# Optimization experiments

Hardware: AMD Instinct MI355X
Metric: run time of the kernel (lower is better)

The kernel has to match this reference:

```python
import jax, jax.numpy as jnp
import numpy as np

B, S, P, D, H, L, DFF = 4, 2048, 32, 512, 8, 2, 2048
HD = D // H
NV = 8  # number of variates; S = NV * 256 patches
SCALE = 1.0 / np.sqrt(HD)


def _rope_tables(seq_len, dim, base=10000.0):
    inv = 1.0 / (base ** (jnp.arange(0, dim, 2, dtype=jnp.float32) / dim))
    freqs = jnp.outer(jnp.arange(seq_len, dtype=jnp.float32), inv)  # (S, dim/2)
    emb = jnp.concatenate([freqs, freqs], axis=-1)  # (S, dim)
    return jnp.cos(emb), jnp.sin(emb)


def _apply_rope(x, cos, sin):
    # x: (..., S, HD); cos/sin: (S, HD)
    x1, x2 = x[..., ::2], x[..., 1::2]
    ch, sh = cos[..., ::2], sin[..., ::2]
    r1 = x1 * ch - x2 * sh
    r2 = x1 * sh + x2 * ch
    return jnp.stack([r1, r2], axis=-1).reshape(x.shape)


def _ln(x, g, b, eps=1e-5):
    m = x.mean(-1, keepdims=True)
    v = x.var(-1, keepdims=True)
    return (x - m) / jnp.sqrt(v + eps) * g + b


def setup_inputs() -> dict:
    key = jax.random.key(0)
    ks = jax.random.split(key, 20)
    s = 0.02
    x = jax.random.normal(ks[0], (B, S, P), dtype=jnp.float32)
    # 8 variates, 256 patches each, flattened: [0]*256, [1]*256, ...
    variate_ids = jnp.broadcast_to(jnp.arange(S, dtype=jnp.int32) // (S // NV), (B, S))
    mask = jnp.ones((B, S), dtype=jnp.float32)
    f32 = jnp.float32
    return {
        'x': x, 'variate_ids': variate_ids, 'mask': mask,
        'W_pe': jax.random.normal(ks[1], (P, D), f32) * s, 'b_pe': jnp.zeros((D,), f32),
        'Wq': jax.random.normal(ks[2], (L, D, D), f32) * s, 'bq': jnp.zeros((L, D), f32),
        'Wk': jax.random.normal(ks[3], (L, D, D), f32) * s, 'bk': jnp.zeros((L, D), f32),
        'Wv': jax.random.normal(ks[4], (L, D, D), f32) * s, 'bv': jnp.zeros((L, D), f32),
        'Wo': jax.random.normal(ks[5], (L, D, D), f32) * s, 'bo': jnp.zeros((L, D), f32),
        'u_same': jax.random.normal(ks[6], (L, H), f32) * 0.1,
        'u_cross': jax.random.normal(ks[7], (L, H), f32) * 0.1,
        'g1': jnp.ones((L, D), f32), 'be1': jnp.zeros((L, D), f32),
        'W1': jax.random.normal(ks[8], (L, D, DFF), f32) * s, 'b1f': jnp.zeros((L, DFF), f32),
        'W2': jax.random.normal(ks[9], (L, DFF, D), f32) * s, 'b2f': jnp.zeros((L, D), f32),
        'g2': jnp.ones((L, D), f32), 'be2': jnp.zeros((L, D), f32),
        'Wh': jax.random.normal(ks[10], (D, P), f32) * s, 'bh': jnp.zeros((P,), f32),
    }


def reference(x, variate_ids, mask, W_pe, b_pe, Wq, bq, Wk, bk, Wv, bv, Wo, bo,
              u_same, u_cross, g1, be1, W1, b1f, W2, b2f, g2, be2, Wh, bh):
    b, s, _ = x.shape
    h = x @ W_pe + b_pe  # patch embedding: (B,S,D)
    cos, sin = _rope_tables(s, HD)
    same = (variate_ids[:, :, None] == variate_ids[:, None, :]).astype(h.dtype)  # (B,S,S)
    mask_add = (1.0 - mask)[:, None, None, :] * -1e9  # (B,1,1,S)
    for l in range(L):
        q = (h @ Wq[l] + bq[l]).reshape(b, s, H, HD).transpose(0, 2, 1, 3)
        k = (h @ Wk[l] + bk[l]).reshape(b, s, H, HD).transpose(0, 2, 1, 3)
        v = (h @ Wv[l] + bv[l]).reshape(b, s, H, HD).transpose(0, 2, 1, 3)
        q = _apply_rope(q, cos, sin)
        k = _apply_rope(k, cos, sin)
        scores = jnp.einsum('bhqd,bhkd->bhqk', q, k) * SCALE
        bias = (same[:, None] * u_same[l][None, :, None, None]
                + (1.0 - same)[:, None] * u_cross[l][None, :, None, None])
        scores = scores + bias + mask_add
        p = jax.nn.softmax(scores, axis=-1)
        o = jnp.einsum('bhqk,bhkd->bhqd', p, v).transpose(0, 2, 1, 3).reshape(b, s, D)
        o = o @ Wo[l] + bo[l]
        h = _ln(h + o, g1[l], be1[l])
        f = jax.nn.gelu(h @ W1[l] + b1f[l], approximate=False) @ W2[l] + b2f[l]
        h = _ln(h + f, g2[l], be2[l])
    return h @ Wh + bh  # forecasting head: (B,S,P)
```

## Files before the change

### kernel.cpp

```cpp
#include <hip/hip_runtime.h>

typedef unsigned short u16;
typedef unsigned int   u32;
typedef __attribute__((ext_vector_type(8))) short bf16x8;
typedef __attribute__((ext_vector_type(4))) short bf16x4;
typedef __attribute__((ext_vector_type(4))) float f32x4;
typedef __attribute__((ext_vector_type(4))) int   i32x4;

constexpr int B_ = 4, S_ = 2048, D_ = 512, H_ = 8, L_ = 2, DFF_ = 2048;
constexpr int BS_ = B_ * S_;
constexpr float QSC_ = 0.18033688011f;
constexpr float LOG2E_ = 1.44269504089f;

__device__ __forceinline__ u16 f2bf(float f) {
    u32 u = __float_as_uint(f);
    u += 0x7fffu + ((u >> 16) & 1u);
    return (u16)(u >> 16);
}
__device__ __forceinline__ float bf2f(u16 u) {
    return __uint_as_float(((u32)u) << 16);
}
__device__ __forceinline__ u32 cvt_pk_bf16(float lo, float hi) {
    u32 d;
    asm volatile("v_cvt_pk_bf16_f32 %0, %1, %2" : "=v"(d) : "v"(lo), "v"(hi));
    return d;
}
__device__ __forceinline__ float exp2v(float x) {
    float d;
    asm("v_exp_f32 %0, %1" : "=v"(d) : "v"(x));
    return d;
}

__global__ __launch_bounds__(256)
void wtrans_all(const float* __restrict__ Wpe, const float* __restrict__ Wq,
                const float* __restrict__ Wk, const float* __restrict__ Wv,
                const float* __restrict__ Wo, const float* __restrict__ W1,
                const float* __restrict__ W2, const float* __restrict__ Whd,
                u16* __restrict__ wpe_t, u16* __restrict__ whd_t,
                u16* __restrict__ wbase)
{
    __shared__ float tile[32][33];
    int id = blockIdx.x;
    const float* src; u16* dst; int K, N, tx, ty;
    if (id < 16) {
        src = Wpe; dst = wpe_t; K = 32; N = 512; tx = id; ty = 0;
    } else if (id >= 6160) {
        src = Whd; dst = whd_t; K = 512; N = 32; tx = 0; ty = id - 6160;
    } else {
        id -= 16;
        if (id < 2048) {
            int mat = id >> 8, l = mat >> 2, w = mat & 3;
            const float* srcs[4] = { Wq, Wk, Wv, Wo };
            src = srcs[w] + (size_t)l * 262144;
            u16* base = wbase + (size_t)l * 3145728;
            dst = base + (size_t)w * 262144;
            K = 512; N = 512;
            int t8 = id & 255; tx = t8 & 15; ty = t8 >> 4;
        } else if (id < 4096) {
            id -= 2048;
            int l = id >> 10, t = id & 1023;
            src = W1 + (size_t)l * 1048576;
            dst = wbase + (size_t)l * 3145728 + 1048576;
            K = 512; N = 2048; tx = t & 63; ty = t >> 6;
        } else {
            id -= 4096;
            int l = id >> 10, t = id & 1023;
            src = W2 + (size_t)l * 1048576;
            dst = wbase + (size_t)l * 3145728 + 2097152;
            K = 2048; N = 512; tx = t & 15; ty = t >> 4;
        }
    }
    const int n0 = tx * 32, k0 = ty * 32;
    const int t = threadIdx.x;
#pragma unroll
    for (int i = 0; i < 4; i++) {
        int lin = i * 256 + t;
        int r = lin >> 5, c = lin & 31;
        tile[r][c] = src[(size_t)(k0 + r) * N + n0 + c];
    }
    __syncthreads();
#pragma unroll
    for (int i = 0; i < 4; i++) {
        int lin = i * 256 + t;
        int r = lin >> 5, c = lin & 31;
        dst[(size_t)(n0 + r) * K + k0 + c] = f2bf(tile[c][r]);
    }
}

__global__ __launch_bounds__(256)
void misc_prep(const float* __restrict__ x, u16* __restrict__ xb,
               const float* __restrict__ bq, const float* __restrict__ bk,
               const float* __restrict__ bv, float* __restrict__ bqkv,
               float* __restrict__ rc, float* __restrict__ rs)
{
    const int id = blockIdx.x, t = threadIdx.x;
    if (id < 256) {
        int idx = id * 256 + t;
        int j = idx & 31, tpos = idx >> 5;
        float inv = __expf(-(float)j * 0.28782313662425572f);
        float ang = (float)tpos * inv;
        rc[idx] = cosf(ang);
        rs[idx] = sinf(ang);
    } else if (id < 512) {
        int i = (id - 256) * 256 + t;
        float4 f = *reinterpret_cast<const float4*>(x + (size_t)i * 4);
        uint2 pk;
        pk.x = (u32)f2bf(f.x) | ((u32)f2bf(f.y) << 16);
        pk.y = (u32)f2bf(f.z) | ((u32)f2bf(f.w) << 16);
        *reinterpret_cast<uint2*>(xb + (size_t)i * 4) = pk;
    } else {
        int idx = (id - 512) * 256 + t;
        if (idx < L_ * 1536) {
            int l = idx / 1536, i = idx % 1536;
            float v = (i < 512) ? bq[l * 512 + i]
                    : (i < 1024) ? bk[l * 512 + i - 512]
                                 : bv[l * 512 + i - 1024];
            bqkv[idx] = v;
        }
    }
}

template<int ACT, int BN, int ROPE>
__global__ __launch_bounds__(256)
void gemm_kernel(const u16* __restrict__ A, const u16* __restrict__ Bt,
                 const float* __restrict__ bias, u16* __restrict__ C,
                 int M, int N, int K, int lda,
                 u16* __restrict__ qd, u16* __restrict__ kd, u16* __restrict__ vd,
                 const float* __restrict__ rc, const float* __restrict__ rs)
{
    constexpr int LDT = 40;
    constexpr int NI = BN / 32;
    __shared__ u16 As[128 * LDT];
    __shared__ u16 Bs[BN * LDT];
    const int t = threadIdx.x;
    const int m0 = blockIdx.y * 128, n0 = blockIdx.x * BN;
    const int lane = t & 63, w = t >> 6;
    const int wr = w >> 1, wc = w & 1;
    const int l15 = lane & 15, lhi = lane >> 4;

    f32x4 acc[4][NI];
#pragma unroll
    for (int i = 0; i < 4; i++)
#pragma unroll
        for (int j = 0; j < NI; j++)
#pragma unroll
            for (int r = 0; r < 4; r++) acc[i][j][r] = 0.f;

    for (int kt = 0; kt < K; kt += 32) {
#pragma unroll
        for (int i = 0; i < 2; i++) {
            int lin = i * 256 + t;
            int r = lin >> 2, c8 = (lin & 3) << 3;
            *reinterpret_cast<bf16x8*>(&As[r * LDT + c8]) =
                *reinterpret_cast<const bf16x8*>(A + (size_t)(m0 + r) * lda + kt + c8);
        }
#pragma unroll
        for (int i = 0; i < BN / 64; i++) {
            int lin = i * 256 + t;
            int r = lin >> 2, c8 = (lin & 3) << 3;
            *reinterpret_cast<bf16x8*>(&Bs[r * LDT + c8]) =
                *reinterpret_cast<const bf16x8*>(Bt + (size_t)(n0 + r) * K + kt + c8);
        }
        __syncthreads();
        bf16x8 af[4], bfv[NI];
#pragma unroll
        for (int mi = 0; mi < 4; mi++)
            af[mi] = *reinterpret_cast<const bf16x8*>(&As[(wr * 64 + mi * 16 + l15) * LDT + lhi * 8]);
#pragma unroll
        for (int ni = 0; ni < NI; ni++)
            bfv[ni] = *reinterpret_cast<const bf16x8*>(&Bs[(wc * (BN / 2) + ni * 16 + l15) * LDT + lhi * 8]);
#pragma unroll
        for (int mi = 0; mi < 4; mi++)
#pragma unroll
            for (int ni = 0; ni < NI; ni++)
                acc[mi][ni] = __builtin_amdgcn_mfma_f32_16x16x32_bf16(af[mi], bfv[ni], acc[mi][ni], 0, 0, 0);
        __syncthreads();
    }

    float bb[NI];
#pragma unroll
    for (int ni = 0; ni < NI; ni++) bb[ni] = bias[n0 + wc * (BN / 2) + ni * 16 + l15];
#pragma unroll
    for (int mi = 0; mi < 4; mi++) {
        int row = m0 + wr * 64 + mi * 16 + lhi * 4;
#pragma unroll
        for (int ni = 0; ni < NI; ni++) {
            int col = n0 + wc * (BN / 2) + ni * 16 + l15;
#pragma unroll
            for (int r = 0; r < 4; r++) {
                float v = acc[mi][ni][r] + bb[ni];
                if (ACT == 1) v = 0.5f * v * (1.0f + erff(v * 0.70710678118654752f));
                C[(size_t)(row + r) * N + col] = f2bf(v);
            }
        }
    }
}

template<int ACT, int BN, int ROPE>
__global__ __launch_bounds__(256)
void gemm_db(const u16* __restrict__ A, const u16* __restrict__ Bt,
             const float* __restrict__ bias, u16* __restrict__ C,
             int M, int N, int K, int lda,
             u16* __restrict__ qd, u16* __restrict__ kd, u16* __restrict__ vd,
             const float* __restrict__ rc, const float* __restrict__ rs)
{
    constexpr int NI = BN / 32;
    constexpr int ABYTES = 128 * 128;
    constexpr int BBYTES = BN * 128;
    constexpr int HALF = ABYTES + BBYTES;
    __shared__ char lds[2 * HALF];
    const int t = threadIdx.x;
    const int m0 = blockIdx.y * 128, n0 = blockIdx.x * BN;
    const int lane = t & 63, w = t >> 6;
    const int wr = w >> 1, wc = w & 1;
    const int l15 = lane & 15, lhi = lane >> 4;
    const int sw = (l15 & 7) << 4;

    auto stage = [&](int kt, int buf) {
        char* base = lds + buf * HALF;
#pragma unroll
        for (int p = 0; p < ABYTES / 4096; p++) {
            int off = p * 4096 + t * 16;
            int so = off ^ (((off >> 7) & 7) << 4);
            int row = off >> 7;
            int col = (so & 127) >> 1;
            __builtin_amdgcn_global_load_lds(
                (const __attribute__((address_space(1))) void*)(A + (size_t)(m0 + row) * lda + kt + col),
                (__attribute__((address_space(3))) void*)(base + off), 16, 0, 0);
        }
        char* bb = base + ABYTES;
#pragma unroll
        for (int p = 0; p < BBYTES / 4096; p++) {
            int off = p * 4096 + t * 16;
            int so = off ^ (((off >> 7) & 7) << 4);
            int row = off >> 7;
            int col = (so & 127) >> 1;
            __builtin_amdgcn_global_load_lds(
                (const __attribute__((address_space(1))) void*)(Bt + (size_t)(n0 + row) * K + kt + col),
                (__attribute__((address_space(3))) void*)(bb + off), 16, 0, 0);
        }
    };

    f32x4 acc[4][NI];
#pragma unroll
    for (int i = 0; i < 4; i++)
#pragma unroll
        for (int j = 0; j < NI; j++)
#pragma unroll
            for (int r = 0; r < 4; r++) acc[i][j][r] = 0.f;

    stage(0, 0);
    int buf = 0;
    for (int kt = 0; kt < K; kt += 64) {
        if (kt + 64 < K) {
            stage(kt + 64, buf ^ 1);
            if constexpr (BN == 64) asm volatile("s_waitcnt vmcnt(6)" ::: "memory");
            else                    asm volatile("s_waitcnt vmcnt(8)" ::: "memory");
        } else {
            asm volatile("s_waitcnt vmcnt(0)" ::: "memory");
        }
        __builtin_amdgcn_s_barrier();
        const char* La = lds + buf * HALF;
        const char* Lb = La + ABYTES;
        bf16x8 af[4][2], bfv[NI][2];
#pragma unroll
        for (int mi = 0; mi < 4; mi++) {
            int row = wr * 64 + mi * 16 + l15;
#pragma unroll
            for (int kk = 0; kk < 2; kk++)
                af[mi][kk] = *reinterpret_cast<const bf16x8*>(La + ((row * 128 + kk * 64 + lhi * 16) ^ sw));
        }
#pragma unroll
        for (int ni = 0; ni < NI; ni++) {
            int row = wc * (BN / 2) + ni * 16 + l15;
#pragma unroll
            for (int kk = 0; kk < 2; kk++)
                bfv[ni][kk] = *reinterpret_cast<const bf16x8*>(Lb + ((row * 128 + kk * 64 + lhi * 16) ^ sw));
        }
        __builtin_amdgcn_s_setprio(1);
#pragma unroll
        for (int kk = 0; kk < 2; kk++)
#pragma unroll
            for (int mi = 0; mi < 4; mi++)
#pragma unroll
                for (int ni = 0; ni < NI; ni++)
                    acc[mi][ni] = __builtin_amdgcn_mfma_f32_16x16x32_bf16(af[mi][kk], bfv[ni][kk], acc[mi][ni], 0, 0, 0);
        __builtin_amdgcn_s_setprio(0);
        __builtin_amdgcn_s_barrier();
        buf ^= 1;
    }

    float bb[NI];
#pragma unroll
    for (int ni = 0; ni < NI; ni++) bb[ni] = bias[n0 + wc * (BN / 2) + ni * 16 + l15];

    if (ROPE == 0) {
#pragma unroll
        for (int mi = 0; mi < 4; mi++) {
            int row = m0 + wr * 64 + mi * 16 + lhi * 4;
#pragma unroll
            for (int ni = 0; ni < NI; ni++) {
                int col = n0 + wc * (BN / 2) + ni * 16 + l15;
#pragma unroll
                for (int r = 0; r < 4; r++) {
                    float v = acc[mi][ni][r] + bb[ni];
                    if (ACT == 1) v = 0.5f * v * (1.0f + erff(v * 0.70710678118654752f));
                    C[(size_t)(row + r) * N + col] = f2bf(v);
                }
            }
        }
    } else {
#pragma unroll
        for (int ni = 0; ni < NI; ni++) {
            int colb = n0 + wc * (BN / 2) + ni * 16;
            int region = colb >> 9;
            int col = colb + l15;
            int d = col & 63;
            int head = (col >> 6) & 7;
#pragma unroll
            for (int mi = 0; mi < 4; mi++) {
                int row0 = m0 + wr * 64 + mi * 16 + lhi * 4;
                int sp0 = row0 & (S_ - 1);
                int bidx0 = row0 >> 11;
                if (region == 2) {
                    float vv[4];
#pragma unroll
                    for (int r = 0; r < 4; r++) vv[r] = acc[mi][ni][r] + bb[ni];
                    uint2 pk;
                    pk.x = (u32)f2bf(vv[0]) | ((u32)f2bf(vv[1]) << 16);
                    pk.y = (u32)f2bf(vv[2]) | ((u32)f2bf(vv[3]) << 16);
                    *reinterpret_cast<uint2*>(vd + (((size_t)(bidx0 * 8 + head) * 64 + d) << 11) + sp0) = pk;
                } else {
#pragma unroll
                    for (int r = 0; r < 4; r++) {
                        int sp = sp0 + r;
                        float v = acc[mi][ni][r] + bb[ni];
                        float px = __shfl_xor(v, 1);
                        int f = d & 30;
                        float cs = rc[sp * 32 + f], sn = rs[sp * 32 + f];
                        float ov = (l15 & 1) ? fmaf(px, sn, v * cs)
                                             : fmaf(v, cs, -(px * sn));
                        if (region == 0) ov *= QSC_;
                        u16* dst = (region == 0) ? qd : kd;
                        dst[((size_t)(bidx0 * 8 + head) * S_ + sp) * 64 + d] = f2bf(ov);
                    }
                }
            }
        }
    }
}

__global__ __launch_bounds__(512, 4)
void attn_kernel(const u16* __restrict__ qbp, const u16* __restrict__ kbp,
                 const u16* __restrict__ vt, const int* __restrict__ vid,
                 const float* __restrict__ maskp,
                 const float* __restrict__ usame, const float* __restrict__ ucross,
                 u16* __restrict__ o)
{
    __shared__ u16 ldsK[3][64 * 64];
    __shared__ u16 ldsV[3][64 * 64];
    __shared__ int   vids[S_];
    __shared__ float cbase[S_];
    const int bidx = blockIdx.x;
    const int xcd = bidx & 7;
    const int j = bidx >> 3;
    const int bh = xcd * 4 + (j >> 4);
    const int chunk = j & 15;
    const int b = bh >> 3, hh = bh & 7;
    const int t = threadIdx.x;
    const int lane = t & 63, wid = t >> 6;
    const int q0 = chunk * 128 + wid * 16;
    const int l15 = lane & 15, lhi = lane >> 4;
    const int sw = (l15 & 7) << 4;
    const int ssw = ((t >> 3) & 7) << 4;
    const u16* qp = qbp + (size_t)bh * S_ * 64;
    const u16* kp = kbp + (size_t)bh * S_ * 64;
    const u16* vp = vt + (size_t)bh * 64 * S_;
    const float us = usame[hh] * LOG2E_, uc = ucross[hh] * LOG2E_;
    const float df = us - uc;
    const int* vidb = vid + (size_t)b * S_;
    const float* mkb = maskp + (size_t)b * S_;
    const bf16x4 ones = { (short)0x3F80, (short)0x3F80, (short)0x3F80, (short)0x3F80 };

    bf16x8 qfr[2];
#pragma unroll
    for (int kk = 0; kk < 2; kk++)
        qfr[kk] = *reinterpret_cast<const bf16x8*>(
            qp + (size_t)(q0 + l15) * 64 + kk * 32 + lhi * 8);

    {
        i32x4 vv = reinterpret_cast<const i32x4*>(vidb)[t];
        f32x4 mm = reinterpret_cast<const f32x4*>(mkb)[t];
        f32x4 cb;
#pragma unroll
        for (int r = 0; r < 4; r++) cb[r] = fmaf(1.0f - mm[r], -1.44269504e9f, uc);
        reinterpret_cast<i32x4*>(vids)[t] = vv;
        reinterpret_cast<f32x4*>(cbase)[t] = cb;
    }

    auto stage = [&](int tile, int buf) {
        const char* kg = (const char*)kp + (size_t)tile * 8192;
        {
            int off = t * 16;
            int so = off ^ ssw;
            __builtin_amdgcn_global_load_lds(
                (const __attribute__((address_space(1))) void*)(kg + so),
                (__attribute__((address_space(3))) void*)((char*)&ldsK[buf][0] + off), 16, 0, 0);
        }
        const char* vg = (const char*)vp + (size_t)tile * 128;
        {
            int off = t * 16;
            int so = off ^ ssw;
            int row = so >> 7, colb = so & 127;
            __builtin_amdgcn_global_load_lds(
                (const __attribute__((address_space(1))) void*)(vg + (size_t)row * 4096 + colb),
                (__attribute__((address_space(3))) void*)((char*)&ldsV[buf][0] + off), 16, 0, 0);
        }
    };

    stage(0, 0);
    stage(1, 1);
    asm volatile("s_waitcnt vmcnt(2) lgkmcnt(0)" ::: "memory");
    __builtin_amdgcn_s_barrier();

    const int vq = vids[q0 + l15];

    float mrow = -1e30f;
    f32x4 lacc;
    f32x4 oT[4];
#pragma unroll
    for (int r = 0; r < 4; r++) lacc[r] = 0.f;
#pragma unroll
    for (int nd = 0; nd < 4; nd++)
#pragma unroll
        for (int r = 0; r < 4; r++) oT[nd][r] = 0.f;

    constexpr int NT = S_ / 64;

    auto qk = [&](int buf, int tile, f32x4 (&sx)[4]) {
        const u16* Kb = ldsK[buf];
        const int kv0 = tile * 64;
        __builtin_amdgcn_s_setprio(1);
#pragma unroll
        for (int ni = 0; ni < 4; ni++) {
            f32x4 cb = *reinterpret_cast<const f32x4*>(&cbase[kv0 + ni * 16 + lhi * 4]);
            int rowb = (ni * 16 + l15) * 128;
            bf16x8 kf0 = *reinterpret_cast<const bf16x8*>((const char*)Kb + ((rowb + lhi * 16) ^ sw));
            bf16x8 kf1 = *reinterpret_cast<const bf16x8*>((const char*)Kb + ((rowb + 64 + lhi * 16) ^ sw));
            sx[ni] = __builtin_amdgcn_mfma_f32_16x16x32_bf16(kf0, qfr[0], cb, 0, 0, 0);
            sx[ni] = __builtin_amdgcn_mfma_f32_16x16x32_bf16(kf1, qfr[1], sx[ni], 0, 0, 0);
        }
        __builtin_amdgcn_s_setprio(0);
    };

    auto finish = [&](int tt, int buf, f32x4 (&sx)[4]) {
        const int kv0 = tt * 64;
#pragma unroll
        for (int ni = 0; ni < 4; ni++) {
            i32x4 vkq = *reinterpret_cast<const i32x4*>(&vids[kv0 + ni * 16 + lhi * 4]);
#pragma unroll
            for (int r = 0; r < 4; r++)
                sx[ni][r] += (vkq[r] == vq) ? df : 0.f;
        }
        float pm = sx[0][0];
#pragma unroll
        for (int ni = 0; ni < 4; ni++)
#pragma unroll
            for (int r = 0; r < 4; r++)
                if (ni || r) pm = fmaxf(pm, sx[ni][r]);
        pm = fmaxf(pm, __shfl_xor(pm, 16));
        pm = fmaxf(pm, __shfl_xor(pm, 32));
        if (!__all(pm <= mrow + 8.f)) {
            float mnew = fmaxf(mrow, pm);
            float alpha = exp2v(mrow - mnew);
            mrow = mnew;
#pragma unroll
            for (int r = 0; r < 4; r++) lacc[r] *= alpha;
#pragma unroll
            for (int nd = 0; nd < 4; nd++)
#pragma unroll
                for (int r = 0; r < 4; r++) oT[nd][r] *= alpha;
        }
        bf16x4 pb[4];
#pragma unroll
        for (int ni = 0; ni < 4; ni++) {
            float p0 = exp2v(sx[ni][0] - mrow);
            float p1 = exp2v(sx[ni][1] - mrow);
            float p2 = exp2v(sx[ni][2] - mrow);
            float p3 = exp2v(sx[ni][3] - mrow);
            union { u32 u[2]; bf16x4 h; } uu;
            uu.u[0] = cvt_pk_bf16(p0, p1);
            uu.u[1] = cvt_pk_bf16(p2, p3);
            pb[ni] = uu.h;
        }
        const u16* Vb = ldsV[buf];
        __builtin_amdgcn_s_setprio(1);
#pragma unroll
        for (int ni = 0; ni < 4; ni++)
            lacc = __builtin_amdgcn_mfma_f32_16x16x16bf16_1k(ones, pb[ni], lacc, 0, 0, 0);
#pragma unroll
        for (int nd = 0; nd < 4; nd++) {
            int rowb = (nd * 16 + l15) * 128;
#pragma unroll
            for (int ni = 0; ni < 4; ni++) {
                bf16x4 vf = *reinterpret_cast<const bf16x4*>((const char*)Vb + ((rowb + ni * 32 + lhi * 8) ^ sw));
                oT[nd] = __builtin_amdgcn_mfma_f32_16x16x16bf16_1k(vf, pb[ni], oT[nd], 0, 0, 0);
            }
        }
        __builtin_amdgcn_s_setprio(0);
    };

    f32x4 s0[4], s1[4];
    qk(0, 0, s0);

    auto step = [&](int u, f32x4 (&sA)[4], f32x4 (&sB)[4]) {
        if (u + 2 < NT) stage(u + 2, (u + 2) % 3);
        if (u + 1 < NT) {
            if (u + 2 < NT) asm volatile("s_waitcnt vmcnt(2)" ::: "memory");
            else            asm volatile("s_waitcnt vmcnt(0)" ::: "memory");
            __builtin_amdgcn_s_barrier();
            qk((u + 1) % 3, u + 1, sB);
        }
        finish(u, u % 3, sA);
        __builtin_amdgcn_s_barrier();
    };

    for (int tt = 0; tt < NT; tt += 2) {
        step(tt, s0, s1);
        step(tt + 1, s1, s0);
    }

    {
        float inv = 1.0f / lacc[0];
        size_t rowb = (size_t)(b * S_ + q0 + l15) * D_;
#pragma unroll
        for (int nd = 0; nd < 4; nd++) {
            uint2 st;
            st.x = cvt_pk_bf16(oT[nd][0] * inv, oT[nd][1] * inv);
            st.y = cvt_pk_bf16(oT[nd][2] * inv, oT[nd][3] * inv);
            *reinterpret_cast<uint2*>(o + rowb + hh * 64 + nd * 16 + lhi * 4) = st;
        }
    }
}

__global__ __launch_bounds__(256)
void ln_kernel(u16* hb, const u16* __restrict__ tb,
               const float* __restrict__ g, const float* __restrict__ be)
{
    const int row = blockIdx.x * 4 + (threadIdx.x >> 6);
    const int lane = threadIdx.x & 63;
    u16* hp = hb + (size_t)row * D_ + lane * 8;
    const u16* tp = tb + (size_t)row * D_ + lane * 8;
    bf16x8 a = *reinterpret_cast<const bf16x8*>(hp);
    bf16x8 c = *reinterpret_cast<const bf16x8*>(tp);
    float x[8];
    float s = 0.f, s2 = 0.f;
#pragma unroll
    for (int j = 0; j < 8; j++) {
        x[j] = bf2f((u16)a[j]) + bf2f((u16)c[j]);
        s += x[j]; s2 += x[j] * x[j];
    }
#pragma unroll
    for (int m = 1; m <= 32; m <<= 1) { s += __shfl_xor(s, m); s2 += __shfl_xor(s2, m); }
    float mean = s * (1.0f / 512.0f);
    float var = s2 * (1.0f / 512.0f) - mean * mean;
    float rstd = rsqrtf(var + 1e-5f);
    const float* gp = g + lane * 8;
    const float* bp = be + lane * 8;
    bf16x8 ov;
#pragma unroll
    for (int j = 0; j < 8; j++)
        ov[j] = (short)f2bf((x[j] - mean) * rstd * gp[j] + bp[j]);
    *reinterpret_cast<bf16x8*>(hp) = ov;
}

__global__ __launch_bounds__(256)
void head_mfma(const u16* __restrict__ hb, const u16* __restrict__ wht,
               const float* __restrict__ bhv, float* __restrict__ out)
{
    __shared__ u16 Bs[32 * 520];
    const int t = threadIdx.x;
#pragma unroll
    for (int i = 0; i < 8; i++) {
        int idx = i * 256 + t;
        int n = idx >> 6, kc = idx & 63;
        *reinterpret_cast<bf16x8*>(&Bs[n * 520 + kc * 8]) =
            reinterpret_cast<const bf16x8*>(wht)[idx];
    }
    __syncthreads();
    const int lane = t & 63, w = t >> 6;
    const int l15 = lane & 15, lhi = lane >> 4;
    const int row0 = blockIdx.x * 128 + w * 32;

    f32x4 acc[2][2];
#pragma unroll
    for (int mi = 0; mi < 2; mi++)
#pragma unroll
        for (int ni = 0; ni < 2; ni++)
#pragma unroll
            for (int r = 0; r < 4; r++) acc[mi][ni][r] = 0.f;

#pragma unroll 4
    for (int kt = 0; kt < 512; kt += 32) {
        bf16x8 af[2], bf[2];
#pragma unroll
        for (int mi = 0; mi < 2; mi++)
            af[mi] = *reinterpret_cast<const bf16x8*>(
                hb + (size_t)(row0 + mi * 16 + l15) * 512 + kt + lhi * 8);
#pragma unroll
        for (int ni = 0; ni < 2; ni++)
            bf[ni] = *reinterpret_cast<const bf16x8*>(&Bs[(ni * 16 + l15) * 520 + kt + lhi * 8]);
#pragma unroll
        for (int mi = 0; mi < 2; mi++)
#pragma unroll
            for (int ni = 0; ni < 2; ni++)
                acc[mi][ni] = __builtin_amdgcn_mfma_f32_16x16x32_bf16(af[mi], bf[ni], acc[mi][ni], 0, 0, 0);
    }
#pragma unroll
    for (int mi = 0; mi < 2; mi++)
#pragma unroll
        for (int ni = 0; ni < 2; ni++) {
            int col = ni * 16 + l15;
            float bv = bhv[col];
#pragma unroll
            for (int r = 0; r < 4; r++)
                out[(size_t)(row0 + mi * 16 + lhi * 4 + r) * 32 + col] = acc[mi][ni][r] + bv;
        }
}

extern "C" void kernel_launch(void* const* d_in, const int* in_sizes, int n_in,
                              void* d_out, int out_size, void* d_ws, size_t ws_size,
                              hipStream_t stream)
{
    (void)in_sizes; (void)n_in; (void)out_size; (void)ws_size;
    const float* x     = (const float*)d_in[0];
    const int*   vid   = (const int*)d_in[1];
    const float* maskp = (const float*)d_in[2];
    const float* Wpe   = (const float*)d_in[3];
    const float* bpe   = (const float*)d_in[4];
    const float* Wq    = (const float*)d_in[5];
    const float* bq    = (const float*)d_in[6];
    const float* Wk    = (const float*)d_in[7];
    const float* bk    = (const float*)d_in[8];
    const float* Wv    = (const float*)d_in[9];
    const float* bv    = (const float*)d_in[10];
    const float* Wo    = (const float*)d_in[11];
    const float* bo    = (const float*)d_in[12];
    const float* usame = (const float*)d_in[13];
    const float* ucros = (const float*)d_in[14];
    const float* g1    = (const float*)d_in[15];
    const float* be1   = (const float*)d_in[16];
    const float* W1    = (const float*)d_in[17];
    const float* b1f   = (const float*)d_in[18];
    const float* W2    = (const float*)d_in[19];
    const float* b2f   = (const float*)d_in[20];
    const float* g2    = (const float*)d_in[21];
    const float* be2   = (const float*)d_in[22];
    const float* Whd   = (const float*)d_in[23];
    const float* bhd   = (const float*)d_in[24];

    constexpr size_t MB = 1024ull * 1024ull;
    char* ws = (char*)d_ws;
    u16*   hb   = (u16*)(ws + 0);
    u16*   qbb  = (u16*)(ws + 8 * MB);
    u16*   kbb  = (u16*)(ws + 16 * MB);
    u16*   vtb  = (u16*)(ws + 24 * MB);
    u16*   ob   = (u16*)(ws + 40 * MB);
    u16*   tb   = (u16*)(ws + 48 * MB);
    u16*   fb   = (u16*)(ws + 56 * MB);
    u16*   xb   = (u16*)(ws + 88 * MB);
    float* rc   = (float*)(ws + 89 * MB);
    float* rs   = (float*)(ws + 89 * MB + 262144);
    float* bqkv = (float*)(ws + 90 * MB);
    u16*   wpe_t = (u16*)(ws + 91 * MB);
    u16*   whd_t = (u16*)(ws + 91 * MB + 65536);
    u16*   wbase = (u16*)(ws + 92 * MB);

    auto qkvt = [&](int l) { return wbase + (size_t)l * 3145728; };
    auto wot  = [&](int l) { return qkvt(l) + 786432; };
    auto w1t  = [&](int l) { return qkvt(l) + 1048576; };
    auto w2t  = [&](int l) { return qkvt(l) + 2097152; };

    wtrans_all<<<6176, 256, 0, stream>>>(Wpe, Wq, Wk, Wv, Wo, W1, W2, Whd,
                                         wpe_t, whd_t, wbase);
    misc_prep<<<524, 256, 0, stream>>>(x, xb, bq, bk, bv, bqkv, rc, rs);

    gemm_kernel<0, 64, 0><<<dim3(8, 64), 256, 0, stream>>>(
        xb, wpe_t, bpe, hb, BS_, 512, 32, 32,
        (u16*)nullptr, (u16*)nullptr, (u16*)nullptr, (const float*)nullptr, (const float*)nullptr);

    for (int l = 0; l < L_; l++) {
        gemm_db<0, 128, 1><<<dim3(12, 64), 256, 0, stream>>>(
            hb, qkvt(l), bqkv + l * 1536, (u16*)nullptr, BS_, 1536, 512, 512,
            qbb, kbb, vtb, rc, rs);
        attn_kernel<<<512, 512, 0, stream>>>(qbb, kbb, vtb, vid, maskp,
                                             usame + l * H_, ucros + l * H_, ob);
        gemm_db<0, 128, 0><<<dim3(4, 64), 256, 0, stream>>>(
            ob, wot(l), bo + l * 512, tb, BS_, 512, 512, 512,
            (u16*)nullptr, (u16*)nullptr, (u16*)nullptr, (const float*)nullptr, (const float*)nullptr);
        ln_kernel<<<2048, 256, 0, stream>>>(hb, tb, g1 + l * 512, be1 + l * 512);
        gemm_db<1, 128, 0><<<dim3(16, 64), 256, 0, stream>>>(
            hb, w1t(l), b1f + l * 2048, fb, BS_, 2048, 512, 512,
            (u16*)nullptr, (u16*)nullptr, (u16*)nullptr, (const float*)nullptr, (const float*)nullptr);
        gemm_db<0, 128, 0><<<dim3(4, 64), 256, 0, stream>>>(
            fb, w2t(l), b2f + l * 512, tb, BS_, 512, 2048, 2048,
            (u16*)nullptr, (u16*)nullptr, (u16*)nullptr, (const float*)nullptr, (const float*)nullptr);
        ln_kernel<<<2048, 256, 0, stream>>>(hb, tb, g2 + l * 512, be2 + l * 512);
    }
    head_mfma<<<64, 256, 0, stream>>>(hb, whd_t, bhd, (float*)d_out);
}
```

Measured before the change: 357.2 us.

## Restructure GEMM and attention pipelines to drop barriers, add max3 and split row-sum

```diff
diff --git a/kernel.cpp b/kernel.cpp
--- a/kernel.cpp
+++ b/kernel.cpp
@@ -28,6 +28,11 @@
 __device__ __forceinline__ float exp2v(float x) {
     float d;
     asm("v_exp_f32 %0, %1" : "=v"(d) : "v"(x));
+    return d;
+}
+__device__ __forceinline__ float max3v(float a, float b, float c) {
+    float d;
+    asm("v_max3_f32 %0, %1, %2, %3" : "=v"(d) : "v"(a), "v"(b), "v"(c));
     return d;
 }
 
@@ -252,13 +257,7 @@
     stage(0, 0);
     int buf = 0;
     for (int kt = 0; kt < K; kt += 64) {
-        if (kt + 64 < K) {
-            stage(kt + 64, buf ^ 1);
-            if constexpr (BN == 64) asm volatile("s_waitcnt vmcnt(6)" ::: "memory");
-            else                    asm volatile("s_waitcnt vmcnt(8)" ::: "memory");
-        } else {
-            asm volatile("s_waitcnt vmcnt(0)" ::: "memory");
-        }
+        asm volatile("s_waitcnt vmcnt(0)" ::: "memory");
         __builtin_amdgcn_s_barrier();
         const char* La = lds + buf * HALF;
         const char* Lb = La + ABYTES;
@@ -277,6 +276,7 @@
             for (int kk = 0; kk < 2; kk++)
                 bfv[ni][kk] = *reinterpret_cast<const bf16x8*>(Lb + ((row * 128 + kk * 64 + lhi * 16) ^ sw));
         }
+        if (kt + 64 < K) stage(kt + 64, buf ^ 1);
         __builtin_amdgcn_s_setprio(1);
 #pragma unroll
         for (int kk = 0; kk < 2; kk++)
@@ -286,7 +286,6 @@
                 for (int ni = 0; ni < NI; ni++)
                     acc[mi][ni] = __builtin_amdgcn_mfma_f32_16x16x32_bf16(af[mi][kk], bfv[ni][kk], acc[mi][ni], 0, 0, 0);
         __builtin_amdgcn_s_setprio(0);
-        __builtin_amdgcn_s_barrier();
         buf ^= 1;
     }
 
@@ -357,8 +356,8 @@
                  const float* __restrict__ usame, const float* __restrict__ ucross,
                  u16* __restrict__ o)
 {
-    __shared__ u16 ldsK[3][64 * 64];
-    __shared__ u16 ldsV[3][64 * 64];
+    __shared__ u16 ldsK[4][64 * 64];
+    __shared__ u16 ldsV[4][64 * 64];
     __shared__ int   vids[S_];
     __shared__ float cbase[S_];
     const int bidx = blockIdx.x;
@@ -423,13 +422,11 @@
     asm volatile("s_waitcnt vmcnt(2) lgkmcnt(0)" ::: "memory");
     __builtin_amdgcn_s_barrier();
 
-    const int vq = vids[q0 + l15];
-
     float mrow = -1e30f;
-    f32x4 lacc;
+    f32x4 la, lb;
     f32x4 oT[4];
 #pragma unroll
-    for (int r = 0; r < 4; r++) lacc[r] = 0.f;
+    for (int r = 0; r < 4; r++) { la[r] = 0.f; lb[r] = 0.f; }
 #pragma unroll
     for (int nd = 0; nd < 4; nd++)
 #pragma unroll
@@ -453,6 +450,8 @@
         __builtin_amdgcn_s_setprio(0);
     };
 
+    const int vq = vidb[q0 + l15];
+
     auto finish = [&](int tt, int buf, f32x4 (&sx)[4]) {
         const int kv0 = tt * 64;
 #pragma unroll
@@ -462,12 +461,12 @@
             for (int r = 0; r < 4; r++)
                 sx[ni][r] += (vkq[r] == vq) ? df : 0.f;
         }
-        float pm = sx[0][0];
-#pragma unroll
-        for (int ni = 0; ni < 4; ni++)
-#pragma unroll
-            for (int r = 0; r < 4; r++)
-                if (ni || r) pm = fmaxf(pm, sx[ni][r]);
+        float a0 = max3v(sx[0][0], sx[0][1], sx[0][2]);
+        float a1 = max3v(sx[0][3], sx[1][0], sx[1][1]);
+        float a2 = max3v(sx[1][2], sx[1][3], sx[2][0]);
+        float a3 = max3v(sx[2][1], sx[2][2], sx[2][3]);
+        float a4 = max3v(sx[3][0], sx[3][1], sx[3][2]);
+        float pm = fmaxf(max3v(a0, a1, a2), max3v(a3, a4, sx[3][3]));
         pm = fmaxf(pm, __shfl_xor(pm, 16));
         pm = fmaxf(pm, __shfl_xor(pm, 32));
         if (!__all(pm <= mrow + 8.f)) {
@@ -475,7 +474,7 @@
             float alpha = exp2v(mrow - mnew);
             mrow = mnew;
 #pragma unroll
-            for (int r = 0; r < 4; r++) lacc[r] *= alpha;
+            for (int r = 0; r < 4; r++) { la[r] *= alpha; lb[r] *= alpha; }
 #pragma unroll
             for (int nd = 0; nd < 4; nd++)
 #pragma unroll
@@ -495,9 +494,10 @@
         }
         const u16* Vb = ldsV[buf];
         __builtin_amdgcn_s_setprio(1);
-#pragma unroll
-        for (int ni = 0; ni < 4; ni++)
-            lacc = __builtin_amdgcn_mfma_f32_16x16x16bf16_1k(ones, pb[ni], lacc, 0, 0, 0);
+        la = __builtin_amdgcn_mfma_f32_16x16x16bf16_1k(ones, pb[0], la, 0, 0, 0);
+        lb = __builtin_amdgcn_mfma_f32_16x16x16bf16_1k(ones, pb[1], lb, 0, 0, 0);
+        la = __builtin_amdgcn_mfma_f32_16x16x16bf16_1k(ones, pb[2], la, 0, 0, 0);
+        lb = __builtin_amdgcn_mfma_f32_16x16x16bf16_1k(ones, pb[3], lb, 0, 0, 0);
 #pragma unroll
         for (int nd = 0; nd < 4; nd++) {
             int rowb = (nd * 16 + l15) * 128;
@@ -514,15 +514,15 @@
     qk(0, 0, s0);
 
     auto step = [&](int u, f32x4 (&sA)[4], f32x4 (&sB)[4]) {
-        if (u + 2 < NT) stage(u + 2, (u + 2) % 3);
-        if (u + 1 < NT) {
-            if (u + 2 < NT) asm volatile("s_waitcnt vmcnt(2)" ::: "memory");
-            else            asm volatile("s_waitcnt vmcnt(0)" ::: "memory");
-            __builtin_amdgcn_s_barrier();
-            qk((u + 1) % 3, u + 1, sB);
-        }
-        finish(u, u % 3, sA);
+        if (u + 2 < NT) {
+            stage(u + 2, (u + 2) & 3);
+            asm volatile("s_waitcnt vmcnt(2)" ::: "memory");
+        } else {
+            asm volatile("s_waitcnt vmcnt(0)" ::: "memory");
+        }
         __builtin_amdgcn_s_barrier();
+        if (u + 1 < NT) qk((u + 1) & 3, u + 1, sB);
+        finish(u, u & 3, sA);
     };
 
     for (int tt = 0; tt < NT; tt += 2) {
@@ -531,7 +531,7 @@
     }
 
     {
-        float inv = 1.0f / lacc[0];
+        float inv = 1.0f / (la[0] + lb[0]);
         size_t rowb = (size_t)(b * S_ + q0 + l15) * D_;
 #pragma unroll
         for (int nd = 0; nd < 4; nd++) {
```

After: 374.9 us. 4.9% more time.
